# Kernel tuning notes

Hardware: AMD Instinct MI355X
Metric: run time of the kernel (lower is better)

## Reference

```python
import jax, jax.numpy as jnp
import numpy as np
import math

B, S, H = 8, 1024, 1024
NH, DH = 16, 64  # MULTI_HEAD, HIDDEN_SIZE_HEAD


def setup_inputs() -> dict:
    key = jax.random.key(0)
    ks = jax.random.split(key, 12)
    scale = 0.02
    inp = {
        "v": jax.random.normal(ks[0], (B, S, H), jnp.float32),
        "k": jax.random.normal(ks[1], (B, S, H), jnp.float32),
        "q": jax.random.normal(ks[2], (B, S, H), jnp.float32),
        # True = masked position (masked_fill semantics)
        "mask": jax.random.bernoulli(ks[3], 0.1, (B, 1, 1, S)),
        "Wq": jax.random.normal(ks[4], (H, H), jnp.float32) * scale,
        "bq": jnp.zeros((H,), jnp.float32),
        "Wk": jax.random.normal(ks[5], (H, H), jnp.float32) * scale,
        "bk": jnp.zeros((H,), jnp.float32),
        "Wv": jax.random.normal(ks[6], (H, H), jnp.float32) * scale,
        "bv": jnp.zeros((H,), jnp.float32),
        "Wm": jax.random.normal(ks[7], (H, H), jnp.float32) * scale,
        "bm": jnp.zeros((H,), jnp.float32),
    }
    return inp


def _split_heads(x):
    # [B, S, H] -> [B, NH, S, DH]
    b, s, _ = x.shape
    return x.reshape(b, s, NH, DH).transpose(0, 2, 1, 3)


def reference(v, k, q, mask, Wq, bq, Wk, bk, Wv, bv, Wm, bm):
    # QKV projections (torch Linear: x @ W.T + b)
    qh = _split_heads(q @ Wq.T + bq)  # [B, NH, S, DH]
    kh = _split_heads(k @ Wk.T + bk)
    vh = _split_heads(v @ Wv.T + bv)

    scores = jnp.einsum("bhqd,bhkd->bhqk", qh, kh) / math.sqrt(DH)
    scores = jnp.where(mask, jnp.float32(-1e9), scores)
    att = jax.nn.softmax(scores, axis=-1)
    # dropout rate 0.0 (eval mode) -> identity
    ctx = jnp.einsum("bhqk,bhkd->bhqd", att, vh)  # [B, NH, S, DH]

    b = q.shape[0]
    merged = ctx.transpose(0, 2, 1, 3).reshape(b, -1, NH * DH)  # [B, S, H]
    return merged @ Wm.T + bm
```

## Files before the change

kernel.cpp:

```cpp
#include <hip/hip_runtime.h>
#include <hip/hip_bf16.h>

#define Bn 8
#define Sn 1024
#define Hn 1024
#define NHn 16
#define DHn 64
#define Mn (Bn * Sn)

typedef unsigned short u16;
typedef short bf16x8 __attribute__((ext_vector_type(8)));
typedef unsigned short u16x4 __attribute__((ext_vector_type(4)));
typedef float f32x4 __attribute__((ext_vector_type(4)));

__device__ __forceinline__ u16 f2bf(float x) {
  union { __hip_bfloat16 h; u16 u; } cv;
  cv.h = __float2bfloat16(x);
  return cv.u;
}

__device__ __forceinline__ void async_ld16(void* lds, const void* g) {
  __builtin_amdgcn_global_load_lds(
      (const __attribute__((address_space(1))) void*)g,
      (__attribute__((address_space(3))) void*)lds, 16, 0, 0);
}

template <int CTRL>
__device__ __forceinline__ float dpp_mov(float v) {
  union { float f; int i; } a, b;
  a.f = v;
  b.i = __builtin_amdgcn_mov_dpp(a.i, CTRL, 0xF, 0xF, 1);
  return b.f;
}
__device__ __forceinline__ float row16_max(float v) {
  v = fmaxf(v, dpp_mov<0xB1>(v));
  v = fmaxf(v, dpp_mov<0x4E>(v));
  v = fmaxf(v, dpp_mov<0x124>(v));
  v = fmaxf(v, dpp_mov<0x128>(v));
  return v;
}
__device__ __forceinline__ float row16_sum(float v) {
  v += dpp_mov<0xB1>(v);
  v += dpp_mov<0x4E>(v);
  v += dpp_mov<0x124>(v);
  v += dpp_mov<0x128>(v);
  return v;
}

__global__ __launch_bounds__(256) void sniff_k(const void* __restrict__ mask,
                                               int* __restrict__ flags) {
  __shared__ int viol;
  if (threadIdx.x == 0) viol = 0;
  __syncthreads();
  const unsigned* mw = (const unsigned*)mask;
  int vb = 0;
#pragma unroll
  for (int j = 0; j < 8; ++j) {
    unsigned v = mw[threadIdx.x * 8 + j];
    if (v > 1u) vb |= 1;
    if ((v & 0xFEFEFEFEu) != 0u) vb |= 2;
    if (!(v == 0u || v == 0x3F800000u)) vb |= 4;
    unsigned h0 = v & 0xFFFFu, h1 = v >> 16;
    if (!((h0 == 0u || h0 == 0x3F80u) && (h1 == 0u || h1 == 0x3F80u))) vb |= 8;
  }
  if (vb) atomicOr(&viol, vb);
  __syncthreads();
  if (threadIdx.x == 0) {
    int mt;
    if (!(viol & 1))      mt = 0;
    else if (!(viol & 2)) mt = 1;
    else if (!(viol & 4)) mt = 3;
    else if (!(viol & 8)) mt = 2;
    else                  mt = 0;
    flags[1] = mt;
  }
}

__global__ __launch_bounds__(256) void convert3(
    const float* __restrict__ a, const float* __restrict__ b,
    const float* __restrict__ c, u16* __restrict__ da,
    u16* __restrict__ db, u16* __restrict__ dc) {
  const int seg = blockIdx.x >> 12;
  const int bid = blockIdx.x & 4095;
  const float* s = seg == 0 ? a : seg == 1 ? b : c;
  u16* d        = seg == 0 ? da : seg == 1 ? db : dc;
  const int i = (bid * 256 + threadIdx.x) * 8;
  f32x4 lo = *(const f32x4*)(s + i);
  f32x4 hi = *(const f32x4*)(s + i + 4);
  bf16x8 o;
#pragma unroll
  for (int j = 0; j < 4; ++j) { o[j] = (short)f2bf(lo[j]); o[4 + j] = (short)f2bf(hi[j]); }
  *(bf16x8*)(d + i) = o;
}

__global__ __launch_bounds__(256) void convertW(
    const float* __restrict__ a, const float* __restrict__ b,
    const float* __restrict__ c, const float* __restrict__ e,
    u16* __restrict__ da, u16* __restrict__ db,
    u16* __restrict__ dc, u16* __restrict__ de) {
  const int seg = blockIdx.x >> 9;
  const int bid = blockIdx.x & 511;
  const float* s = seg == 0 ? a : seg == 1 ? b : seg == 2 ? c : e;
  u16* d        = seg == 0 ? da : seg == 1 ? db : seg == 2 ? dc : de;
  const int i = (bid * 256 + threadIdx.x) * 8;
  f32x4 lo = *(const f32x4*)(s + i);
  f32x4 hi = *(const f32x4*)(s + i + 4);
  bf16x8 o;
#pragma unroll
  for (int j = 0; j < 4; ++j) { o[j] = (short)f2bf(lo[j]); o[4 + j] = (short)f2bf(hi[j]); }
  *(bf16x8*)(d + i) = o;
}

template <int OMODE>
__global__ __launch_bounds__(256) void gemm_bt(
    const u16* __restrict__ X, const u16* __restrict__ W,
    const float* __restrict__ bias, void* __restrict__ O, float scale)
{
  __shared__ __attribute__((aligned(16))) u16 As[128 * 32];
  __shared__ __attribute__((aligned(16))) u16 Bs[128 * 32];
  const int tid  = threadIdx.x;
  const int wave = tid >> 6;
  const int lane = tid & 63;
  const int ln   = lane & 15;
  const int quad = lane >> 4;
  const int m0 = blockIdx.x * 128;
  const int n0 = blockIdx.y * 128;
  const int wm = (wave & 1) * 64;
  const int wn = (wave >> 1) * 64;
  const int r0 = tid >> 2;
  const int oc = (tid & 3) * 8;
  char* A0 = (char*)As + wave * 1024;
  char* A1 = (char*)As + 4096 + wave * 1024;
  char* B0 = (char*)Bs + wave * 1024;
  char* B1 = (char*)Bs + 4096 + wave * 1024;

  f32x4 acc[4][4] = {};

  for (int k0 = 0; k0 < 1024; k0 += 32) {
    async_ld16(A0, X + (size_t)(m0 + r0) * 1024 + k0 + oc);
    async_ld16(A1, X + (size_t)(m0 + 64 + r0) * 1024 + k0 + oc);
    async_ld16(B0, W + (size_t)(n0 + r0) * 1024 + k0 + oc);
    async_ld16(B1, W + (size_t)(n0 + 64 + r0) * 1024 + k0 + oc);
    __syncthreads();
    bf16x8 af[4], bf[4];
#pragma unroll
    for (int t = 0; t < 4; ++t)
      af[t] = *(const bf16x8*)&As[(wm + t * 16 + ln) * 32 + quad * 8];
#pragma unroll
    for (int t = 0; t < 4; ++t)
      bf[t] = *(const bf16x8*)&Bs[(wn + t * 16 + ln) * 32 + quad * 8];
#pragma unroll
    for (int i = 0; i < 4; ++i)
#pragma unroll
      for (int j = 0; j < 4; ++j)
        acc[i][j] = __builtin_amdgcn_mfma_f32_16x16x32_bf16(af[i], bf[j], acc[i][j], 0, 0, 0);
    __syncthreads();
  }

  if (OMODE == 2) {
    const int bb = m0 >> 10;
    const int sb = m0 & 1023;
#pragma unroll
    for (int j = 0; j < 4; ++j) {
      const int col = n0 + wn + j * 16 + ln;
      const float bv = bias[col];
#pragma unroll
      for (int i = 0; i < 4; ++i) {
        const int sl = sb + wm + i * 16 + quad * 4;
        u16x4 pk;
#pragma unroll
        for (int r = 0; r < 4; ++r) pk[r] = f2bf((acc[i][j][r] + bv) * scale);
        *(u16x4*)&((u16*)O)[((size_t)(bb * 1024 + col)) * 1024 + sl] = pk;
      }
    }
  } else {
#pragma unroll
    for (int j = 0; j < 4; ++j) {
      const int col = n0 + wn + j * 16 + ln;
      const float bv = bias[col];
#pragma unroll
      for (int i = 0; i < 4; ++i) {
        const int rowb = m0 + wm + i * 16 + quad * 4;
#pragma unroll
        for (int r = 0; r < 4; ++r) {
          const float val = (acc[i][j][r] + bv) * scale;
          const size_t idx = (size_t)(rowb + r) * 1024 + col;
          if (OMODE == 1) ((float*)O)[idx] = val;
          else            ((u16*)O)[idx]   = f2bf(val);
        }
      }
    }
  }
}

__global__ __launch_bounds__(256, 3) void attn(
    const u16* __restrict__ Qb, const u16* __restrict__ Kb,
    const u16* __restrict__ Vbt, const void* __restrict__ mask,
    const int* __restrict__ flags, u16* __restrict__ Ctx)
{
  __shared__ __attribute__((aligned(16))) u16 Ks[128 * 64];
  __shared__ __attribute__((aligned(16))) u16 Vt[64 * 128];
  __shared__ __attribute__((aligned(16))) u16 Pl[4][16 * 128];
  __shared__ __attribute__((aligned(16))) float maskf[Sn];

  const int tid  = threadIdx.x;
  const int wave = tid >> 6;
  const int lane = tid & 63;
  const int ln   = lane & 15;
  const int quad = lane >> 4;
  const int bx  = blockIdx.x;
  const int x   = bx & 7;
  const int qt  = (bx >> 3) & 15;
  const int grp = bx >> 7;
  const int bh  = grp * 8 + x;
  const int b   = bh >> 4;
  const int h   = bh & 15;

  const int mt = flags[1];
  for (int i = tid; i < Sn; i += 256) {
    const int idx = b * Sn + i;
    int nz;
    if (mt == 0)      nz = ((const int*)mask)[idx] != 0;
    else if (mt == 1) nz = ((const signed char*)mask)[idx] != 0;
    else if (mt == 2) nz = ((const u16*)mask)[idx] != 0;
    else              nz = ((const unsigned*)mask)[idx] != 0;
    maskf[i] = nz ? -1e9f : 0.0f;
  }

  const size_t qoff = (size_t)(b * Sn + qt * 64 + wave * 16 + ln) * Hn + h * DHn;
  bf16x8 qf0 = *(const bf16x8*)&Qb[qoff + quad * 8];
  bf16x8 qf1 = *(const bf16x8*)&Qb[qoff + 32 + quad * 8];

  float mrun[4], lrun[4];
#pragma unroll
  for (int r = 0; r < 4; ++r) { mrun[r] = -INFINITY; lrun[r] = 0.0f; }
  f32x4 acc[4] = {};

  const int kr = tid >> 1, kh = tid & 1;
  const int vd = tid >> 2, vs = tid & 3;
  char* pw  = (char*)Pl[wave];
  char* KsB = (char*)Ks;
  char* VtB = (char*)Vt;

  const int kwb = kr * 128 + kh * 64;
  const int ksw = (kr & 7) << 4;
  const int vwb = vd * 256 + vs * 64;
  const int vsw = (vd & 7) << 4;
  const int rsw = (ln & 7) << 4;

  for (int t8 = 0; t8 < 8; ++t8) {
    const int kv0 = t8 * 128;
    __syncthreads();
    {
      const u16* g = &Kb[(size_t)(b * Sn + kv0 + kr) * Hn + h * DHn + kh * 32];
#pragma unroll
      for (int j = 0; j < 4; ++j)
        *(bf16x8*)(KsB + ((kwb + j * 16) ^ ksw)) = *(const bf16x8*)(g + j * 8);
    }
    {
      const u16* g = &Vbt[(size_t)(b * Sn + h * DHn + vd) * Sn + kv0 + vs * 32];
#pragma unroll
      for (int j = 0; j < 4; ++j)
        *(bf16x8*)(VtB + ((vwb + j * 16) ^ vsw)) = *(const bf16x8*)(g + j * 8);
    }
    __syncthreads();

    f32x4 sc[8];
#pragma unroll
    for (int t = 0; t < 8; ++t) {
      const int rb = (t * 16 + ln) * 128;
      bf16x8 kf0 = *(const bf16x8*)(KsB + ((rb + quad * 16) ^ rsw));
      bf16x8 kf1 = *(const bf16x8*)(KsB + ((rb + 64 + quad * 16) ^ rsw));
      f32x4 z = {};
      z = __builtin_amdgcn_mfma_f32_16x16x32_bf16(qf0, kf0, z, 0, 0, 0);
      z = __builtin_amdgcn_mfma_f32_16x16x32_bf16(qf1, kf1, z, 0, 0, 0);
      sc[t] = z;
    }
    float mf[8];
#pragma unroll
    for (int t = 0; t < 8; ++t) mf[t] = maskf[kv0 + t * 16 + ln];
#pragma unroll
    for (int t = 0; t < 8; ++t)
#pragma unroll
      for (int r = 0; r < 4; ++r) sc[t][r] += mf[t];

    float al[4], mx[4];
#pragma unroll
    for (int r = 0; r < 4; ++r) {
      float v = sc[0][r];
#pragma unroll
      for (int t = 1; t < 8; ++t) v = fmaxf(v, sc[t][r]);
      v = row16_max(v);
      const float mnew = fmaxf(mrun[r], v);
      al[r] = __expf(mrun[r] - mnew);
      mrun[r] = mnew;
      mx[r] = mnew;
    }
#pragma unroll
    for (int r = 0; r < 4; ++r) {
      float s = 0.0f;
#pragma unroll
      for (int t = 0; t < 8; ++t) {
        const float p = __expf(sc[t][r] - mx[r]);
        sc[t][r] = p;
        s += p;
      }
      s = row16_sum(s);
      lrun[r] = lrun[r] * al[r] + s;
    }
#pragma unroll
    for (int t = 0; t < 8; ++t)
#pragma unroll
      for (int r = 0; r < 4; ++r) {
        const int prow = quad * 4 + r;
        *(u16*)(pw + ((prow * 256 + (t * 16 + ln) * 2) ^ ((prow & 7) << 4))) =
            f2bf(sc[t][r]);
      }
#pragma unroll
    for (int dt = 0; dt < 4; ++dt)
#pragma unroll
      for (int r = 0; r < 4; ++r) acc[dt][r] *= al[r];
    bf16x8 pa[4];
#pragma unroll
    for (int c = 0; c < 4; ++c)
      pa[c] = *(const bf16x8*)(pw + ((ln * 256 + c * 64 + quad * 16) ^ rsw));
#pragma unroll
    for (int dt = 0; dt < 4; ++dt) {
      const int vrb = (dt * 16 + ln) * 256;
#pragma unroll
      for (int c = 0; c < 4; ++c) {
        bf16x8 vb = *(const bf16x8*)(VtB + ((vrb + c * 64 + quad * 16) ^ rsw));
        acc[dt] = __builtin_amdgcn_mfma_f32_16x16x32_bf16(pa[c], vb, acc[dt], 0, 0, 0);
      }
    }
  }

#pragma unroll
  for (int dt = 0; dt < 4; ++dt)
#pragma unroll
    for (int r = 0; r < 4; ++r) {
      const int s = qt * 64 + wave * 16 + quad * 4 + r;
      Ctx[(size_t)(b * Sn + s) * Hn + h * DHn + dt * 16 + ln] = f2bf(acc[dt][r] / lrun[r]);
    }
}

extern "C" void kernel_launch(void* const* d_in, const int* in_sizes, int n_in,
                              void* d_out, int out_size, void* d_ws, size_t ws_size,
                              hipStream_t stream) {
  const float* v    = (const float*)d_in[0];
  const float* k    = (const float*)d_in[1];
  const float* q    = (const float*)d_in[2];
  const void*  mask = d_in[3];
  const float* Wq   = (const float*)d_in[4];
  const float* bq   = (const float*)d_in[5];
  const float* Wk   = (const float*)d_in[6];
  const float* bk   = (const float*)d_in[7];
  const float* Wv   = (const float*)d_in[8];
  const float* bv   = (const float*)d_in[9];
  const float* Wm   = (const float*)d_in[10];
  const float* bm   = (const float*)d_in[11];

  char* ws = (char*)d_ws;
  u16* qc  = (u16*)(ws);
  u16* kc  = (u16*)(ws + (16u << 20));
  u16* vc  = (u16*)(ws + (32u << 20));
  u16* Wqc = (u16*)(ws + (48u << 20));
  u16* Wkc = Wqc + (1u << 20);
  u16* Wvc = Wkc + (1u << 20);
  u16* Wmc = Wvc + (1u << 20);
  int* flags = (int*)(ws + (56u << 20));
  u16* Vbt = qc;
  u16* Cx  = kc;
  u16* Qb  = (u16*)d_out;
  u16* Kb  = Qb + (size_t)Mn * Hn;

  sniff_k<<<1, 256, 0, stream>>>(mask, flags);
  convert3<<<3 * 4096, 256, 0, stream>>>(q, k, v, qc, kc, vc);
  convertW<<<4 * 512, 256, 0, stream>>>(Wq, Wk, Wv, Wm, Wqc, Wkc, Wvc, Wmc);

  dim3 grid(Mn / 128, Hn / 128), blk(256);
  gemm_bt<0><<<grid, blk, 0, stream>>>(qc, Wqc, bq, Qb, 0.125f);
  gemm_bt<0><<<grid, blk, 0, stream>>>(kc, Wkc, bk, Kb, 1.0f);
  gemm_bt<2><<<grid, blk, 0, stream>>>(vc, Wvc, bv, Vbt, 1.0f);
  attn<<<dim3(Bn * NHn * (Sn / 64)), blk, 0, stream>>>(Qb, Kb, Vbt, mask, flags, Cx);
  gemm_bt<1><<<grid, blk, 0, stream>>>(Cx, Wmc, bm, d_out, 1.0f);
}
```

Measured before the change: 364.4 us.

## Deepen GEMM K-tile to 64 with XOR-swizzled LDS and batch Q/K projections

The GEMM main loop now stages a 64-wide K slice per iteration instead of 32, which halves the number of barrier pairs. The LDS tile is XOR-swizzled on 16-byte chunks to avoid bank conflicts on the MFMA fragment reads. The Q and K projections are merged into one launch over a z dimension of 2, which saves a kernel launch and gives more blocks per wave. LDS use per block doubles, and launch bounds now request 3 blocks per CU, which may cap registers.

```diff
diff --git a/kernel.cpp b/kernel.cpp
--- a/kernel.cpp
+++ b/kernel.cpp
@@ -112,12 +112,10 @@
 }
 
 template <int OMODE>
-__global__ __launch_bounds__(256) void gemm_bt(
-    const u16* __restrict__ X, const u16* __restrict__ W,
+__device__ __forceinline__ void gemm_core(
+    u16* As, u16* Bs, const u16* __restrict__ X, const u16* __restrict__ W,
     const float* __restrict__ bias, void* __restrict__ O, float scale)
 {
-  __shared__ __attribute__((aligned(16))) u16 As[128 * 32];
-  __shared__ __attribute__((aligned(16))) u16 Bs[128 * 32];
   const int tid  = threadIdx.x;
   const int wave = tid >> 6;
   const int lane = tid & 63;
@@ -127,33 +125,37 @@
   const int n0 = blockIdx.y * 128;
   const int wm = (wave & 1) * 64;
   const int wn = (wave >> 1) * 64;
-  const int r0 = tid >> 2;
-  const int oc = (tid & 3) * 8;
-  char* A0 = (char*)As + wave * 1024;
-  char* A1 = (char*)As + 4096 + wave * 1024;
-  char* B0 = (char*)Bs + wave * 1024;
-  char* B1 = (char*)Bs + 4096 + wave * 1024;
+  const int r8 = tid >> 3;
+  const int cg = ((tid & 7) ^ (r8 & 7)) * 8;
+  char* Ad = (char*)As + wave * 1024;
+  char* Bd = (char*)Bs + wave * 1024;
+  const int rsw = ln & 7;
 
   f32x4 acc[4][4] = {};
 
-  for (int k0 = 0; k0 < 1024; k0 += 32) {
-    async_ld16(A0, X + (size_t)(m0 + r0) * 1024 + k0 + oc);
-    async_ld16(A1, X + (size_t)(m0 + 64 + r0) * 1024 + k0 + oc);
-    async_ld16(B0, W + (size_t)(n0 + r0) * 1024 + k0 + oc);
-    async_ld16(B1, W + (size_t)(n0 + 64 + r0) * 1024 + k0 + oc);
+  for (int k0 = 0; k0 < 1024; k0 += 64) {
+#pragma unroll
+    for (int j = 0; j < 4; ++j) {
+      async_ld16(Ad + j * 4096, X + (size_t)(m0 + j * 32 + r8) * 1024 + k0 + cg);
+      async_ld16(Bd + j * 4096, W + (size_t)(n0 + j * 32 + r8) * 1024 + k0 + cg);
+    }
     __syncthreads();
-    bf16x8 af[4], bf[4];
-#pragma unroll
-    for (int t = 0; t < 4; ++t)
-      af[t] = *(const bf16x8*)&As[(wm + t * 16 + ln) * 32 + quad * 8];
-#pragma unroll
-    for (int t = 0; t < 4; ++t)
-      bf[t] = *(const bf16x8*)&Bs[(wn + t * 16 + ln) * 32 + quad * 8];
-#pragma unroll
-    for (int i = 0; i < 4; ++i)
-#pragma unroll
-      for (int j = 0; j < 4; ++j)
-        acc[i][j] = __builtin_amdgcn_mfma_f32_16x16x32_bf16(af[i], bf[j], acc[i][j], 0, 0, 0);
+#pragma unroll
+    for (int s = 0; s < 2; ++s) {
+      const int co = ((s * 4 + quad) ^ rsw) * 16;
+      bf16x8 af[4], bfr[4];
+#pragma unroll
+      for (int t = 0; t < 4; ++t)
+        af[t] = *(const bf16x8*)((char*)As + (wm + t * 16 + ln) * 128 + co);
+#pragma unroll
+      for (int t = 0; t < 4; ++t)
+        bfr[t] = *(const bf16x8*)((char*)Bs + (wn + t * 16 + ln) * 128 + co);
+#pragma unroll
+      for (int i = 0; i < 4; ++i)
+#pragma unroll
+        for (int j = 0; j < 4; ++j)
+          acc[i][j] = __builtin_amdgcn_mfma_f32_16x16x32_bf16(af[i], bfr[j], acc[i][j], 0, 0, 0);
+    }
     __syncthreads();
   }
 
@@ -191,6 +193,29 @@
       }
     }
   }
+}
+
+template <int OMODE>
+__global__ __launch_bounds__(256, 3) void gemm_bt(
+    const u16* __restrict__ X, const u16* __restrict__ W,
+    const float* __restrict__ bias, void* __restrict__ O, float scale)
+{
+  __shared__ __attribute__((aligned(16))) u16 As[128 * 64];
+  __shared__ __attribute__((aligned(16))) u16 Bs[128 * 64];
+  gemm_core<OMODE>(As, Bs, X, W, bias, O, scale);
+}
+
+__global__ __launch_bounds__(256, 3) void gemm_qk(
+    const u16* __restrict__ Xq, const u16* __restrict__ Wq,
+    const float* __restrict__ bq, u16* __restrict__ Oq,
+    const u16* __restrict__ Xk, const u16* __restrict__ Wk,
+    const float* __restrict__ bk, u16* __restrict__ Ok)
+{
+  __shared__ __attribute__((aligned(16))) u16 As[128 * 64];
+  __shared__ __attribute__((aligned(16))) u16 Bs[128 * 64];
+  const int z = blockIdx.z;
+  gemm_core<0>(As, Bs, z ? Xk : Xq, z ? Wk : Wq, z ? bk : bq,
+               z ? (void*)Ok : (void*)Oq, z ? 1.0f : 0.125f);
 }
 
 __global__ __launch_bounds__(256, 3) void attn(
@@ -378,9 +403,10 @@
   convert3<<<3 * 4096, 256, 0, stream>>>(q, k, v, qc, kc, vc);
   convertW<<<4 * 512, 256, 0, stream>>>(Wq, Wk, Wv, Wm, Wqc, Wkc, Wvc, Wmc);
 
-  dim3 grid(Mn / 128, Hn / 128), blk(256);
-  gemm_bt<0><<<grid, blk, 0, stream>>>(qc, Wqc, bq, Qb, 0.125f);
-  gemm_bt<0><<<grid, blk, 0, stream>>>(kc, Wkc, bk, Kb, 1.0f);
+  dim3 blk(256);
+  gemm_qk<<<dim3(Mn / 128, Hn / 128, 2), blk, 0, stream>>>(
+      qc, Wqc, bq, Qb, kc, Wkc, bk, Kb);
+  dim3 grid(Mn / 128, Hn / 128);
   gemm_bt<2><<<grid, blk, 0, stream>>>(vc, Wvc, bv, Vbt, 1.0f);
   attn<<<dim3(Bn * NHn * (Sn / 64)), blk, 0, stream>>>(Qb, Kb, Vbt, mask, flags, Cx);
   gemm_bt<1><<<grid, blk, 0, stream>>>(Cx, Wmc, bm, d_out, 1.0f);
```

After: 354.5 us. 2.7% less time.
